# Optimization experiments

Hardware: AMD Instinct MI355X
Metric: run time of the kernel (lower is better)

## Reference

```python
import jax, jax.numpy as jnp
import numpy as np

B, L, F_DIM, H = 4, 384, 640, 128
K_COULOMB = 332.0
DIELECTRIC = 80.0
BN_EPS = 1e-5

# amino-acid charge table, index order 'ACDEFGHIKLMNPQRSTVWY'
_AA = 'ACDEFGHIKLMNPQRSTVWY'
_CHG = {'D': -1.0, 'E': -1.0, 'K': 1.0, 'R': 1.0, 'H': 0.1}
_TABLE = np.zeros((20, 3), dtype=np.float32)
for _i, _aa in enumerate(_AA):
    c = _CHG.get(_aa, 0.0)
    _TABLE[_i, 0 if c > 0 else (1 if c < 0 else 2)] = 1.0
CHG_TABLE = jnp.asarray(_TABLE)


def _conv1d(x, w, b, pad):
    # x: [N, Cin, L], w: [Cout, Cin, K]
    y = jax.lax.conv_general_dilated(x, w, (1,), [(pad, pad)],
                                     dimension_numbers=('NCH', 'OIH', 'NCH'))
    return y + b[None, :, None]


def setup_inputs() -> dict:
    key = jax.random.key(0)
    ks = jax.random.split(key, 32)
    s = 0.05

    def rn(k, shape):
        return (jax.random.normal(k, shape) * s).astype(jnp.float32)

    inp = {
        'features': jax.random.normal(ks[0], (B, L, F_DIM), dtype=jnp.float32),
        'seq_ids': jax.random.randint(ks[1], (B, L), 0, 20, dtype=jnp.int32),
        'structures': (jax.random.normal(ks[2], (B, L, 3)) * 10.0).astype(jnp.float32),
        # charge predictor: Linear(F,H) -> ReLU -> BN(H) -> Linear(H,H//2) -> ReLU -> Linear(H//2,3) -> Softmax
        'W1': rn(ks[3], (F_DIM, H)), 'b1': jnp.zeros((H,), jnp.float32),
        'gamma': jnp.ones((H,), jnp.float32), 'beta': jnp.zeros((H,), jnp.float32),
        'rmean': jnp.zeros((H,), jnp.float32), 'rvar': jnp.ones((H,), jnp.float32),
        'W2': rn(ks[4], (H, H // 2)), 'b2': jnp.zeros((H // 2,), jnp.float32),
        'W3': rn(ks[5], (H // 2, 3)), 'b3': jnp.zeros((3,), jnp.float32),
        # salt bridge detector: Linear(2F+1,H) -> ReLU -> Linear(H,64) -> ReLU -> Linear(64,1) -> Sigmoid
        'sW1': rn(ks[6], (2 * F_DIM + 1, H)), 'sb1': jnp.zeros((H,), jnp.float32),
        'sW2': rn(ks[7], (H, 64)), 'sb2': jnp.zeros((64,), jnp.float32),
        'sW3': rn(ks[8], (64, 1)), 'sb3': jnp.zeros((1,), jnp.float32),
        # potential calculator convs (OIH layout)
        'c1w': rn(ks[9], (16, 1, 5)), 'c1b': jnp.zeros((16,), jnp.float32),
        'c2w': rn(ks[10], (8, 16, 3)), 'c2b': jnp.zeros((8,), jnp.float32),
        'c3w': rn(ks[11], (1, 8, 3)), 'c3b': jnp.zeros((1,), jnp.float32),
    }
    return inp


def reference(features, seq_ids, structures,
              W1, b1, gamma, beta, rmean, rvar, W2, b2, W3, b3,
              sW1, sb1, sW2, sb2, sW3, sb3,
              c1w, c1b, c2w, c2b, c3w, c3b):
    b_, l_, f_ = features.shape

    # true charges from sequence (one-hot pos/neg/neutral)
    true_charges = CHG_TABLE[seq_ids]                               # [B,L,3]

    # --- charge predictor (BatchNorm in eval mode: running stats) ---
    x = features.reshape(-1, f_)
    h = jax.nn.relu(x @ W1 + b1)
    h = gamma * (h - rmean) / jnp.sqrt(rvar + BN_EPS) + beta
    h = jax.nn.relu(h @ W2 + b2)
    pc = jax.nn.softmax(h @ W3 + b3, axis=-1).reshape(b_, l_, 3)    # [B,L,3]

    net_charge = pc[:, :, 0:1] - pc[:, :, 1:2]                      # [B,L,1]

    # --- electrostatic potential: 1D conv stack on [B,1,L] ---
    p = net_charge.transpose(0, 2, 1)                               # [B,1,L]
    p = jax.nn.relu(_conv1d(p, c1w, c1b, 2))
    p = jax.nn.relu(_conv1d(p, c2w, c2b, 1))
    p = _conv1d(p, c3w, c3b, 1)
    potential = p.transpose(0, 2, 1)                                # [B,L,1]

    # --- pairwise distances ---
    diff = structures[:, :, None, :] - structures[:, None, :, :]    # [B,L,L,3]
    D = jnp.sqrt(jnp.sum(diff * diff, axis=-1) + 1e-12)             # [B,L,L]

    # --- salt bridges: vectorized edge-MLP over all (pos i, neg j) pairs ---
    pos = pc[:, :, 0] > pc[:, :, 2]                                 # [B,L]
    neg = pc[:, :, 1] > pc[:, :, 2]                                 # [B,L]
    a, bb, d = sW1[:f_], sW1[f_:2 * f_], sW1[2 * f_]                # split cat([fi,fj,dist]) @ sW1
    fi = features @ a                                               # [B,L,H]
    fj = features @ bb                                              # [B,L,H]
    hid = jax.nn.relu(fi[:, :, None, :] + fj[:, None, :, :] + D[..., None] * d + sb1)  # [B,L,L,H]
    hid2 = jax.nn.relu(hid @ sW2 + sb2)                             # [B,L,L,64]
    prob = jax.nn.sigmoid((hid2 @ sW3 + sb3)[..., 0])               # [B,L,L]
    q = pos[:, :, None] & neg[:, None, :] & (D < 4.0) & (prob > 0.5)
    salt_bridge_masks = (q | q.transpose(0, 2, 1)).astype(jnp.float32)  # [B,L,L]

    # --- Coulomb energy with distance-dependent dielectric ---
    # dielectric = eps * D / 4 -> e_ij = k * q_i q_j / (eps/4 * D^2)
    qc = pc[:, :, 0] - pc[:, :, 1]                                  # [B,L]
    valid = (D < 15.0) & (D > 0.0)
    triu = jnp.triu(jnp.ones((l_, l_), bool), k=1)[None]
    D_safe = jnp.where(valid, D, 1.0)
    e_ij = K_COULOMB * qc[:, :, None] * qc[:, None, :] / ((DIELECTRIC / 4.0) * D_safe * D_safe)
    energy = jnp.sum(jnp.where(valid & triu, e_ij, 0.0), axis=(1, 2))  # [B]

    return (pc, true_charges, net_charge, potential, salt_bridge_masks, energy)
```

## Files before the change

kernel.cpp:

```cpp
#include <hip/hip_runtime.h>

#define LSEQ 384
#define NROWS 1536
#define FDIM 640
#define HDIM 128
#define PART 196608

#define WS_H1P 0
#define WS_FIP (4*PART)
#define WS_FJP (8*PART)
#define WS_FI  (12*PART)
#define WS_FJ  (13*PART)
#define WS_QC  (14*PART)
#define WS_FLAG (WS_QC + NROWS)

#define OUT_PC    0
#define OUT_TC    4608
#define OUT_NET   9216
#define OUT_POT   10752
#define OUT_MASK  12288
#define OUT_EN    602112

__global__ __launch_bounds__(256) void k_gemm(const float* __restrict__ X,
                                              const float* __restrict__ W1,
                                              const float* __restrict__ sW1,
                                              float* __restrict__ ws,
                                              float* __restrict__ out) {
    __shared__ float As[2 * 32 * 34];
    __shared__ float Bs[2 * 32 * 64];
    const int t = threadIdx.x;
    if (blockIdx.x == 0 && blockIdx.y == 0 && blockIdx.z == 0 && t < 4)
        out[OUT_EN + t] = 0.0f;

    const int m0 = blockIdx.x * 32;
    const int gy = blockIdx.y, kz = blockIdx.z;
    const int mat = gy >> 1, half = gy & 1, n0 = half * 64;
    const float* W = (mat == 0) ? W1 : (mat == 1 ? sW1 : sW1 + 640 * 128);
    float* O = ws + (mat == 0 ? WS_H1P : (mat == 1 ? WS_FIP : WS_FJP)) + kz * PART;

    const int a_r = t >> 3, a_c = (t & 7) * 4;
    const int b_r = t >> 4, b_c = (t & 15) * 4;
    const int tx = (t & 15) * 4, ty = (t >> 4) * 2;
    const int k0 = kz * 160;

    float acc[2][4] = {};

    float4 av  = *(const float4*)&X[(m0 + a_r) * FDIM + k0 + a_c];
    float4 bv0 = *(const float4*)&W[(k0 + b_r) * HDIM + n0 + b_c];
    float4 bv1 = *(const float4*)&W[(k0 + b_r + 16) * HDIM + n0 + b_c];
    As[(a_c + 0) * 34 + a_r] = av.x;
    As[(a_c + 1) * 34 + a_r] = av.y;
    As[(a_c + 2) * 34 + a_r] = av.z;
    As[(a_c + 3) * 34 + a_r] = av.w;
    *(float4*)&Bs[b_r * 64 + b_c]        = bv0;
    *(float4*)&Bs[(b_r + 16) * 64 + b_c] = bv1;
    __syncthreads();

    for (int it = 0; it < 5; it++) {
        const int buf = it & 1;
        if (it < 4) {
            const int kk = k0 + (it + 1) * 32;
            av  = *(const float4*)&X[(m0 + a_r) * FDIM + kk + a_c];
            bv0 = *(const float4*)&W[(kk + b_r) * HDIM + n0 + b_c];
            bv1 = *(const float4*)&W[(kk + b_r + 16) * HDIM + n0 + b_c];
        }
        const float* Ab = As + buf * 1088;
        const float* Bb = Bs + buf * 2048;
#pragma unroll
        for (int k = 0; k < 32; k++) {
            float2 a = *(const float2*)&Ab[k * 34 + ty];
            float4 b = *(const float4*)&Bb[k * 64 + tx];
            acc[0][0] = fmaf(a.x, b.x, acc[0][0]);
            acc[0][1] = fmaf(a.x, b.y, acc[0][1]);
            acc[0][2] = fmaf(a.x, b.z, acc[0][2]);
            acc[0][3] = fmaf(a.x, b.w, acc[0][3]);
            acc[1][0] = fmaf(a.y, b.x, acc[1][0]);
            acc[1][1] = fmaf(a.y, b.y, acc[1][1]);
            acc[1][2] = fmaf(a.y, b.z, acc[1][2]);
            acc[1][3] = fmaf(a.y, b.w, acc[1][3]);
        }
        if (it < 4) {
            float* Aw = As + (buf ^ 1) * 1088;
            float* Bw = Bs + (buf ^ 1) * 2048;
            Aw[(a_c + 0) * 34 + a_r] = av.x;
            Aw[(a_c + 1) * 34 + a_r] = av.y;
            Aw[(a_c + 2) * 34 + a_r] = av.z;
            Aw[(a_c + 3) * 34 + a_r] = av.w;
            *(float4*)&Bw[b_r * 64 + b_c]        = bv0;
            *(float4*)&Bw[(b_r + 16) * 64 + b_c] = bv1;
            __syncthreads();
        }
    }
#pragma unroll
    for (int r = 0; r < 2; r++) {
        float4 v = make_float4(acc[r][0], acc[r][1], acc[r][2], acc[r][3]);
        *(float4*)&O[(m0 + ty + r) * HDIM + n0 + tx] = v;
    }
}

__global__ __launch_bounds__(256) void k_row(float* __restrict__ ws,
                                             const float* __restrict__ b1,
                                             const float* __restrict__ gam,
                                             const float* __restrict__ bet,
                                             const float* __restrict__ rmean,
                                             const float* __restrict__ rvar,
                                             const float* __restrict__ W2,
                                             const float* __restrict__ b2,
                                             const float* __restrict__ W3,
                                             const float* __restrict__ b3,
                                             const int* __restrict__ seq,
                                             float* __restrict__ out) {
    const int t = threadIdx.x, w = t >> 6, lane = t & 63;
    const int row = blockIdx.x * 4 + w;
    const long base = (long)row * 128;
    const float* h1p = ws + WS_H1P;
    const float* fip = ws + WS_FIP;
    const float* fjp = ws + WS_FJP;

    {
        float fi0 = fip[base + lane] + fip[PART + base + lane]
                  + fip[2 * PART + base + lane] + fip[3 * PART + base + lane];
        float fi1 = fip[base + 64 + lane] + fip[PART + base + 64 + lane]
                  + fip[2 * PART + base + 64 + lane] + fip[3 * PART + base + 64 + lane];
        float fj0 = fjp[base + lane] + fjp[PART + base + lane]
                  + fjp[2 * PART + base + lane] + fjp[3 * PART + base + lane];
        float fj1 = fjp[base + 64 + lane] + fjp[PART + base + 64 + lane]
                  + fjp[2 * PART + base + 64 + lane] + fjp[3 * PART + base + 64 + lane];
        ws[WS_FI + base + lane]      = fi0;
        ws[WS_FI + base + 64 + lane] = fi1;
        ws[WS_FJ + base + lane]      = fj0;
        ws[WS_FJ + base + 64 + lane] = fj1;
    }

    float h0 = h1p[base + lane] + h1p[PART + base + lane]
             + h1p[2 * PART + base + lane] + h1p[3 * PART + base + lane];
    float h1 = h1p[base + 64 + lane] + h1p[PART + base + 64 + lane]
             + h1p[2 * PART + base + 64 + lane] + h1p[3 * PART + base + 64 + lane];
    h0 = fmaxf(h0 + b1[lane], 0.0f);
    h1 = fmaxf(h1 + b1[64 + lane], 0.0f);
    h0 = gam[lane]      * (h0 - rmean[lane])      / sqrtf(rvar[lane] + 1e-5f)      + bet[lane];
    h1 = gam[64 + lane] * (h1 - rmean[64 + lane]) / sqrtf(rvar[64 + lane] + 1e-5f) + bet[64 + lane];

    float acc = b2[lane];
#pragma unroll
    for (int cc = 0; cc < 64; cc++) {
        float wv0 = W2[cc * 64 + lane];
        float wv1 = W2[(cc + 64) * 64 + lane];
        float hv0 = __uint_as_float(__builtin_amdgcn_readlane(__float_as_uint(h0), cc));
        float hv1 = __uint_as_float(__builtin_amdgcn_readlane(__float_as_uint(h1), cc));
        acc = fmaf(hv0, wv0, acc);
        acc = fmaf(hv1, wv1, acc);
    }
    float h2 = fmaxf(acc, 0.0f);
    float x0 = h2 * W3[lane * 3 + 0];
    float x1 = h2 * W3[lane * 3 + 1];
    float x2 = h2 * W3[lane * 3 + 2];
#pragma unroll
    for (int o = 32; o > 0; o >>= 1) {
        x0 += __shfl_xor(x0, o, 64);
        x1 += __shfl_xor(x1, o, 64);
        x2 += __shfl_xor(x2, o, 64);
    }
    if (lane == 0) {
        float l0 = x0 + b3[0], l1 = x1 + b3[1], l2 = x2 + b3[2];
        float m = fmaxf(l0, fmaxf(l1, l2));
        float e0 = expf(l0 - m), e1 = expf(l1 - m), e2 = expf(l2 - m);
        float s = e0 + e1 + e2;
        float pc0 = e0 / s, pc1 = e1 / s, pc2 = e2 / s;
        out[OUT_PC + row * 3 + 0] = pc0;
        out[OUT_PC + row * 3 + 1] = pc1;
        out[OUT_PC + row * 3 + 2] = pc2;
        float net = pc0 - pc1;
        out[OUT_NET + row] = net;
        ws[WS_QC + row] = net;
        ((int*)(ws + WS_FLAG))[row] = (pc0 > pc2 ? 1 : 0) | (pc1 > pc2 ? 2 : 0);
        int sid = seq[row];
        float c0 = (sid == 6 || sid == 8 || sid == 14) ? 1.0f : 0.0f;
        float c1 = (sid == 2 || sid == 3) ? 1.0f : 0.0f;
        out[OUT_TC + row * 3 + 0] = c0;
        out[OUT_TC + row * 3 + 1] = c1;
        out[OUT_TC + row * 3 + 2] = (c0 == 0.0f && c1 == 0.0f) ? 1.0f : 0.0f;
    }
}

__device__ __forceinline__ float mlp_eval(const float* __restrict__ fi, const float* __restrict__ fj,
                                          int gi, int gj, float D,
                                          float dv0, float dv1, float sb0, float sb1v,
                                          float b2v, float w3l, const float* w2s, int lane) {
    float fi0 = fi[(long)gi * 128 + lane];
    float fi1 = fi[(long)gi * 128 + 64 + lane];
    float fj0 = fj[(long)gj * 128 + lane];
    float fj1 = fj[(long)gj * 128 + 64 + lane];
    float h0 = fmaxf(fi0 + fj0 + D * dv0 + sb0, 0.0f);
    float h1 = fmaxf(fi1 + fj1 + D * dv1 + sb1v, 0.0f);
    float a0 = 0.0f, a1 = 0.0f;
#pragma unroll
    for (int cc = 0; cc < 64; cc++) {
        float hv0 = __uint_as_float(__builtin_amdgcn_readlane(__float_as_uint(h0), cc));
        float hv1 = __uint_as_float(__builtin_amdgcn_readlane(__float_as_uint(h1), cc));
        a0 = fmaf(hv0, w2s[cc * 64 + lane], a0);
        a1 = fmaf(hv1, w2s[(cc + 64) * 64 + lane], a1);
    }
    float x = fmaxf(a0 + a1 + b2v, 0.0f) * w3l;
#pragma unroll
    for (int o = 32; o > 0; o >>= 1) x += __shfl_xor(x, o, 64);
    return x;
}

__global__ __launch_bounds__(256) void k2(const float* __restrict__ S,
                                          const float* __restrict__ ws,
                                          const float* __restrict__ sW1,
                                          const float* __restrict__ sb1,
                                          const float* __restrict__ sW2,
                                          const float* __restrict__ sb2,
                                          const float* __restrict__ sW3,
                                          const float* __restrict__ sb3,
                                          const float* __restrict__ c1w, const float* __restrict__ c1b,
                                          const float* __restrict__ c2w, const float* __restrict__ c2b,
                                          const float* __restrict__ c3w, const float* __restrict__ c3b,
                                          float* __restrict__ out) {
    __shared__ char smem[40960];
    const int t = threadIdx.x;
    const int bi = blockIdx.x;

    if (bi < 4) {
        float* p0 = (float*)smem;
        float* p1 = p0 + 388;
        float* p2 = p1 + 16 * 386;
        const int b = bi;
        for (int j = t; j < LSEQ; j += 256) p0[j + 2] = out[OUT_NET + b * LSEQ + j];
        if (t < 2) { p0[t] = 0.0f; p0[LSEQ + 2 + t] = 0.0f; }
        if (t < 16) { p1[t * 386] = 0.0f; p1[t * 386 + 385] = 0.0f; }
        if (t < 8)  { p2[t * 386] = 0.0f; p2[t * 386 + 385] = 0.0f; }
        __syncthreads();
        for (int pos = t; pos < LSEQ; pos += 256) {
#pragma unroll
            for (int o = 0; o < 16; o++) {
                float acc = c1b[o];
#pragma unroll
                for (int k = 0; k < 5; k++) acc = fmaf(p0[pos + k], c1w[o * 5 + k], acc);
                p1[o * 386 + pos + 1] = fmaxf(acc, 0.0f);
            }
        }
        __syncthreads();
        for (int pos = t; pos < LSEQ; pos += 256) {
#pragma unroll
            for (int o = 0; o < 8; o++) {
                float acc = c2b[o];
                for (int i = 0; i < 16; i++)
#pragma unroll
                    for (int k = 0; k < 3; k++)
                        acc = fmaf(p1[i * 386 + pos + k], c2w[(o * 16 + i) * 3 + k], acc);
                p2[o * 386 + pos + 1] = fmaxf(acc, 0.0f);
            }
        }
        __syncthreads();
        for (int pos = t; pos < LSEQ; pos += 256) {
            float acc = c3b[0];
            for (int i = 0; i < 8; i++)
#pragma unroll
                for (int k = 0; k < 3; k++)
                    acc = fmaf(p2[i * 386 + pos + k], c3w[i * 3 + k], acc);
            out[OUT_POT + b * LSEQ + pos] = acc;
        }
        return;
    }

    float* sx = (float*)smem;
    float* sy = sx + 384;
    float* sz = sy + 384;
    float* sq = sz + 384;
    unsigned int* clist = (unsigned int*)(sz + 768);
    unsigned char* sf = (unsigned char*)(smem + 7680);
    float* red = (float*)(smem + 8064);
    int* cntL = (int*)(smem + 8080);
    float* w2s = (float*)(smem + 8192);

    const float* qc = ws + WS_QC;
    const int* flags = (const int*)(ws + WS_FLAG);
    const float* fi = ws + WS_FI;
    const float* fj = ws + WS_FJ;

    const int row = bi - 4;
    const int b = row / LSEQ;
    const int i = row - b * LSEQ;

    for (int j = t; j < LSEQ; j += 256) {
        int g = b * LSEQ + j;
        sx[j] = S[g * 3 + 0];
        sy[j] = S[g * 3 + 1];
        sz[j] = S[g * 3 + 2];
        sq[j] = qc[g];
        sf[j] = (unsigned char)flags[g];
    }
    if (t == 0) *cntL = 0;
    __syncthreads();

    const float six = sx[i], siy = sy[i], siz = sz[i], qi = sq[i];
    const int fli = sf[i];
    const bool posi = (fli & 1) != 0, negi = (fli & 2) != 0;
    const int lane = t & 63, w = t >> 6;
    float esum = 0.0f;
    float* mrow = out + OUT_MASK + (long)row * LSEQ;

    for (int j = t; j < LSEQ; j += 256) {
        float dx = __fsub_rn(six, sx[j]);
        float dy = __fsub_rn(siy, sy[j]);
        float dz = __fsub_rn(siz, sz[j]);
        float d2 = __fadd_rn(__fadd_rn(__fmul_rn(dx, dx), __fmul_rn(dy, dy)), __fmul_rn(dz, dz));
        d2 = __fadd_rn(d2, 1e-12f);
        float D = __fsqrt_rn(d2);
        mrow[j] = 0.0f;
        if (j > i && D < 15.0f && D > 0.0f) {
            float num = __fmul_rn(__fmul_rn(332.0f, qi), sq[j]);
            float den = __fmul_rn(__fmul_rn(20.0f, D), D);
            esum += __fdiv_rn(num, den);
        }
        int flj = sf[j];
        bool near = (D < 4.0f);
        bool need1 = near && posi && ((flj & 2) != 0);
        bool need2 = near && negi && ((flj & 1) != 0);
        if (need1 || need2) {
            int p = atomicAdd(cntL, 1);
            clist[p] = (unsigned int)j | (need1 ? 512u : 0u) | (need2 ? 1024u : 0u);
        }
    }
#pragma unroll
    for (int o = 32; o > 0; o >>= 1) esum += __shfl_xor(esum, o, 64);
    if (lane == 0) red[w] = esum;
    __syncthreads();
    if (t == 0) {
        float s = red[0] + red[1] + red[2] + red[3];
        atomicAdd(&out[OUT_EN + b], s);
    }

    int nc = *cntL;
    if (nc == 0) return;

    for (int idx = t; idx < 2048; idx += 256)
        ((float4*)w2s)[idx] = ((const float4*)sW2)[idx];
    const float* dvec = sW1 + 1280 * 128;
    const float dv0 = dvec[lane], dv1 = dvec[lane + 64];
    const float sb0 = sb1[lane], sb1v = sb1[lane + 64];
    const float w3l = sW3[lane];
    const float b2v = sb2[lane];
    const float b3v = sb3[0];
    __syncthreads();

    for (int c = w; c < nc; c += 4) {
        unsigned int e = clist[c];
        int j = (int)(e & 511u);
        bool need1 = (e & 512u) != 0, need2 = (e & 1024u) != 0;
        float dx = __fsub_rn(six, sx[j]);
        float dy = __fsub_rn(siy, sy[j]);
        float dz = __fsub_rn(siz, sz[j]);
        float d2 = __fadd_rn(__fadd_rn(__fmul_rn(dx, dx), __fmul_rn(dy, dy)), __fmul_rn(dz, dz));
        d2 = __fadd_rn(d2, 1e-12f);
        float D = __fsqrt_rn(d2);
        int gi = row, gj = b * LSEQ + j;
        bool hit = false;
        if (need1) {
            float x = mlp_eval(fi, fj, gi, gj, D, dv0, dv1, sb0, sb1v, b2v, w3l, w2s, lane);
            hit = (x + b3v) > 0.0f;
        }
        if (!hit && need2) {
            float x = mlp_eval(fi, fj, gj, gi, D, dv0, dv1, sb0, sb1v, b2v, w3l, w2s, lane);
            hit = (x + b3v) > 0.0f;
        }
        if (hit && lane == 0) mrow[j] = 1.0f;
    }
}

extern "C" void kernel_launch(void* const* d_in, const int* in_sizes, int n_in,
                              void* d_out, int out_size, void* d_ws, size_t ws_size,
                              hipStream_t stream) {
    const float* X     = (const float*)d_in[0];
    const int*   seq   = (const int*)d_in[1];
    const float* S     = (const float*)d_in[2];
    const float* W1    = (const float*)d_in[3];
    const float* b1    = (const float*)d_in[4];
    const float* gam   = (const float*)d_in[5];
    const float* bet   = (const float*)d_in[6];
    const float* rmean = (const float*)d_in[7];
    const float* rvar  = (const float*)d_in[8];
    const float* W2    = (const float*)d_in[9];
    const float* b2    = (const float*)d_in[10];
    const float* W3    = (const float*)d_in[11];
    const float* b3    = (const float*)d_in[12];
    const float* sW1   = (const float*)d_in[13];
    const float* sb1   = (const float*)d_in[14];
    const float* sW2   = (const float*)d_in[15];
    const float* sb2   = (const float*)d_in[16];
    const float* sW3   = (const float*)d_in[17];
    const float* sb3   = (const float*)d_in[18];
    const float* c1w   = (const float*)d_in[19];
    const float* c1b   = (const float*)d_in[20];
    const float* c2w   = (const float*)d_in[21];
    const float* c2b   = (const float*)d_in[22];
    const float* c3w   = (const float*)d_in[23];
    const float* c3b   = (const float*)d_in[24];

    float* out = (float*)d_out;
    float* ws  = (float*)d_ws;

    hipLaunchKernelGGL(k_gemm, dim3(48, 6, 4), dim3(256), 0, stream, X, W1, sW1, ws, out);
    hipLaunchKernelGGL(k_row, dim3(384), dim3(256), 0, stream,
                       ws, b1, gam, bet, rmean, rvar, W2, b2, W3, b3, seq, out);
    hipLaunchKernelGGL(k2, dim3(1540), dim3(256), 0, stream,
                       S, ws, sW1, sb1, sW2, sb2, sW3, sb3,
                       c1w, c1b, c2w, c2b, c3w, c3b, out);
}
```

Baseline: 156.1 us.

## Fuse feature GEMM with per-row charge MLP, drop split-K partials

Replaces the split-K GEMM and the separate row-reduction kernel with one fused kernel. Each block computes full-K 8-row tiles for all 128 columns, staging tiles into LDS with global_load_lds. For the charge-predictor matrix it then runs bias/ReLU/BN, the second layer, and softmax in-block. This removes the partial-sum workspace traffic and one kernel launch. The cost is fewer, longer-running blocks (576 blocks of 128 threads with 20 serial K steps), which may lower parallelism and latency hiding.

```diff
diff --git a/kernel.cpp b/kernel.cpp
--- a/kernel.cpp
+++ b/kernel.cpp
@@ -6,9 +6,6 @@
 #define HDIM 128
 #define PART 196608
 
-#define WS_H1P 0
-#define WS_FIP (4*PART)
-#define WS_FJP (8*PART)
 #define WS_FI  (12*PART)
 #define WS_FJ  (13*PART)
 #define WS_QC  (14*PART)
@@ -21,165 +18,158 @@
 #define OUT_MASK  12288
 #define OUT_EN    602112
 
-__global__ __launch_bounds__(256) void k_gemm(const float* __restrict__ X,
-                                              const float* __restrict__ W1,
-                                              const float* __restrict__ sW1,
-                                              float* __restrict__ ws,
-                                              float* __restrict__ out) {
-    __shared__ float As[2 * 32 * 34];
-    __shared__ float Bs[2 * 32 * 64];
-    const int t = threadIdx.x;
-    if (blockIdx.x == 0 && blockIdx.y == 0 && blockIdx.z == 0 && t < 4)
-        out[OUT_EN + t] = 0.0f;
-
-    const int m0 = blockIdx.x * 32;
-    const int gy = blockIdx.y, kz = blockIdx.z;
-    const int mat = gy >> 1, half = gy & 1, n0 = half * 64;
-    const float* W = (mat == 0) ? W1 : (mat == 1 ? sW1 : sW1 + 640 * 128);
-    float* O = ws + (mat == 0 ? WS_H1P : (mat == 1 ? WS_FIP : WS_FJP)) + kz * PART;
-
-    const int a_r = t >> 3, a_c = (t & 7) * 4;
-    const int b_r = t >> 4, b_c = (t & 15) * 4;
-    const int tx = (t & 15) * 4, ty = (t >> 4) * 2;
-    const int k0 = kz * 160;
-
-    float acc[2][4] = {};
-
-    float4 av  = *(const float4*)&X[(m0 + a_r) * FDIM + k0 + a_c];
-    float4 bv0 = *(const float4*)&W[(k0 + b_r) * HDIM + n0 + b_c];
-    float4 bv1 = *(const float4*)&W[(k0 + b_r + 16) * HDIM + n0 + b_c];
-    As[(a_c + 0) * 34 + a_r] = av.x;
-    As[(a_c + 1) * 34 + a_r] = av.y;
-    As[(a_c + 2) * 34 + a_r] = av.z;
-    As[(a_c + 3) * 34 + a_r] = av.w;
-    *(float4*)&Bs[b_r * 64 + b_c]        = bv0;
-    *(float4*)&Bs[(b_r + 16) * 64 + b_c] = bv1;
+typedef float f4 __attribute__((ext_vector_type(4)));
+
+__device__ __forceinline__ void gl16(const float* g, float* l) {
+    __builtin_amdgcn_global_load_lds((const __attribute__((address_space(1))) float*)g,
+                                     (__attribute__((address_space(3))) float*)l, 16, 0, 0);
+}
+
+__global__ __launch_bounds__(128) void k_fused(const float* __restrict__ X,
+                                               const float* __restrict__ W1,
+                                               const float* __restrict__ sW1,
+                                               const float* __restrict__ b1,
+                                               const float* __restrict__ gam,
+                                               const float* __restrict__ bet,
+                                               const float* __restrict__ rmean,
+                                               const float* __restrict__ rvar,
+                                               const float* __restrict__ W2,
+                                               const float* __restrict__ b2,
+                                               const float* __restrict__ W3,
+                                               const float* __restrict__ b3,
+                                               const int* __restrict__ seq,
+                                               float* __restrict__ ws,
+                                               float* __restrict__ out) {
+    __shared__ __align__(16) float As[2][8][32];
+    __shared__ __align__(16) float Bs[2][32][128];
+
+    const int t   = threadIdx.x;
+    const int bx  = blockIdx.x;
+    const int mat = blockIdx.y;
+    const int m0  = bx * 8;
+    const float* W = (mat == 0) ? W1 : (mat == 1 ? sW1 : sW1 + FDIM * HDIM);
+
+    if (mat == 0 && bx == 0 && t < 4) out[OUT_EN + t] = 0.0f;
+
+    const int lane = t & 63, wv = t >> 6;
+    const int rg = t >> 5, cg = t & 31;
+
+    auto stage = [&](int buf, int kt) {
+        const int k0 = kt * 32;
+        const float* wsrc = W + (long)k0 * HDIM;
+        float* bdst = &Bs[buf][0][0];
+#pragma unroll
+        for (int c = 0; c < 8; c++) {
+            const int idx = c * 2 + wv;
+            gl16(wsrc + idx * 256 + lane * 4, bdst + idx * 256);
+        }
+        if (wv == 0)
+            gl16(X + (long)(m0 + (lane >> 3)) * FDIM + k0 + (lane & 7) * 4,
+                 &As[buf][0][0]);
+    };
+
+    f4 acc0 = {0.f, 0.f, 0.f, 0.f};
+    f4 acc1 = {0.f, 0.f, 0.f, 0.f};
+
+    stage(0, 0);
     __syncthreads();
 
-    for (int it = 0; it < 5; it++) {
-        const int buf = it & 1;
-        if (it < 4) {
-            const int kk = k0 + (it + 1) * 32;
-            av  = *(const float4*)&X[(m0 + a_r) * FDIM + kk + a_c];
-            bv0 = *(const float4*)&W[(kk + b_r) * HDIM + n0 + b_c];
-            bv1 = *(const float4*)&W[(kk + b_r + 16) * HDIM + n0 + b_c];
-        }
-        const float* Ab = As + buf * 1088;
-        const float* Bb = Bs + buf * 2048;
-#pragma unroll
-        for (int k = 0; k < 32; k++) {
-            float2 a = *(const float2*)&Ab[k * 34 + ty];
-            float4 b = *(const float4*)&Bb[k * 64 + tx];
-            acc[0][0] = fmaf(a.x, b.x, acc[0][0]);
-            acc[0][1] = fmaf(a.x, b.y, acc[0][1]);
-            acc[0][2] = fmaf(a.x, b.z, acc[0][2]);
-            acc[0][3] = fmaf(a.x, b.w, acc[0][3]);
-            acc[1][0] = fmaf(a.y, b.x, acc[1][0]);
-            acc[1][1] = fmaf(a.y, b.y, acc[1][1]);
-            acc[1][2] = fmaf(a.y, b.z, acc[1][2]);
-            acc[1][3] = fmaf(a.y, b.w, acc[1][3]);
-        }
-        if (it < 4) {
-            float* Aw = As + (buf ^ 1) * 1088;
-            float* Bw = Bs + (buf ^ 1) * 2048;
-            Aw[(a_c + 0) * 34 + a_r] = av.x;
-            Aw[(a_c + 1) * 34 + a_r] = av.y;
-            Aw[(a_c + 2) * 34 + a_r] = av.z;
-            Aw[(a_c + 3) * 34 + a_r] = av.w;
-            *(float4*)&Bw[b_r * 64 + b_c]        = bv0;
-            *(float4*)&Bw[(b_r + 16) * 64 + b_c] = bv1;
-            __syncthreads();
-        }
-    }
-#pragma unroll
-    for (int r = 0; r < 2; r++) {
-        float4 v = make_float4(acc[r][0], acc[r][1], acc[r][2], acc[r][3]);
-        *(float4*)&O[(m0 + ty + r) * HDIM + n0 + tx] = v;
-    }
-}
-
-__global__ __launch_bounds__(256) void k_row(float* __restrict__ ws,
-                                             const float* __restrict__ b1,
-                                             const float* __restrict__ gam,
-                                             const float* __restrict__ bet,
-                                             const float* __restrict__ rmean,
-                                             const float* __restrict__ rvar,
-                                             const float* __restrict__ W2,
-                                             const float* __restrict__ b2,
-                                             const float* __restrict__ W3,
-                                             const float* __restrict__ b3,
-                                             const int* __restrict__ seq,
-                                             float* __restrict__ out) {
-    const int t = threadIdx.x, w = t >> 6, lane = t & 63;
-    const int row = blockIdx.x * 4 + w;
-    const long base = (long)row * 128;
-    const float* h1p = ws + WS_H1P;
-    const float* fip = ws + WS_FIP;
-    const float* fjp = ws + WS_FJP;
-
-    {
-        float fi0 = fip[base + lane] + fip[PART + base + lane]
-                  + fip[2 * PART + base + lane] + fip[3 * PART + base + lane];
-        float fi1 = fip[base + 64 + lane] + fip[PART + base + 64 + lane]
-                  + fip[2 * PART + base + 64 + lane] + fip[3 * PART + base + 64 + lane];
-        float fj0 = fjp[base + lane] + fjp[PART + base + lane]
-                  + fjp[2 * PART + base + lane] + fjp[3 * PART + base + lane];
-        float fj1 = fjp[base + 64 + lane] + fjp[PART + base + 64 + lane]
-                  + fjp[2 * PART + base + 64 + lane] + fjp[3 * PART + base + 64 + lane];
-        ws[WS_FI + base + lane]      = fi0;
-        ws[WS_FI + base + 64 + lane] = fi1;
-        ws[WS_FJ + base + lane]      = fj0;
-        ws[WS_FJ + base + 64 + lane] = fj1;
-    }
-
-    float h0 = h1p[base + lane] + h1p[PART + base + lane]
-             + h1p[2 * PART + base + lane] + h1p[3 * PART + base + lane];
-    float h1 = h1p[base + 64 + lane] + h1p[PART + base + 64 + lane]
-             + h1p[2 * PART + base + 64 + lane] + h1p[3 * PART + base + 64 + lane];
-    h0 = fmaxf(h0 + b1[lane], 0.0f);
-    h1 = fmaxf(h1 + b1[64 + lane], 0.0f);
-    h0 = gam[lane]      * (h0 - rmean[lane])      / sqrtf(rvar[lane] + 1e-5f)      + bet[lane];
-    h1 = gam[64 + lane] * (h1 - rmean[64 + lane]) / sqrtf(rvar[64 + lane] + 1e-5f) + bet[64 + lane];
-
-    float acc = b2[lane];
+#pragma unroll 2
+    for (int kt = 0; kt < 20; kt++) {
+        const int buf = kt & 1;
+        if (kt < 19) stage(buf ^ 1, kt + 1);
+
+        const float* Ab = &As[buf][0][0];
+        const float* Bb = &Bs[buf][0][0];
+#pragma unroll
+        for (int k4 = 0; k4 < 32; k4 += 4) {
+            f4 a0 = *(const f4*)&Ab[(rg * 2 + 0) * 32 + k4];
+            f4 a1 = *(const f4*)&Ab[(rg * 2 + 1) * 32 + k4];
+#pragma unroll
+            for (int kk = 0; kk < 4; kk++) {
+                f4 bv = *(const f4*)&Bb[(k4 + kk) * 128 + cg * 4];
+                acc0 += a0[kk] * bv;
+                acc1 += a1[kk] * bv;
+            }
+        }
+        __syncthreads();
+    }
+
+    if (mat != 0) {
+        float* O = ws + (mat == 1 ? WS_FI : WS_FJ);
+        *(f4*)&O[(long)(m0 + rg * 2 + 0) * HDIM + cg * 4] = acc0;
+        *(f4*)&O[(long)(m0 + rg * 2 + 1) * HDIM + cg * 4] = acc1;
+        return;
+    }
+
+    float* hs = (float*)Bs;
+    *(f4*)&hs[(rg * 2 + 0) * 128 + cg * 4] = acc0;
+    *(f4*)&hs[(rg * 2 + 1) * 128 + cg * 4] = acc1;
+    __syncthreads();
+
+    const float b1v0 = b1[lane],      b1v1 = b1[lane + 64];
+    const float sc0  = gam[lane]      / sqrtf(rvar[lane] + 1e-5f);
+    const float sc1  = gam[lane + 64] / sqrtf(rvar[lane + 64] + 1e-5f);
+    const float rm0  = rmean[lane],   rm1  = rmean[lane + 64];
+    const float bt0  = bet[lane],     bt1  = bet[lane + 64];
+
+    float h0[4], h1[4];
+#pragma unroll
+    for (int r = 0; r < 4; r++) {
+        const int row = wv * 4 + r;
+        float v0 = fmaxf(hs[row * 128 + lane] + b1v0, 0.0f);
+        float v1 = fmaxf(hs[row * 128 + 64 + lane] + b1v1, 0.0f);
+        h0[r] = (v0 - rm0) * sc0 + bt0;
+        h1[r] = (v1 - rm1) * sc1 + bt1;
+    }
+
+    const float b2v = b2[lane];
+    float a2[4] = {b2v, b2v, b2v, b2v};
 #pragma unroll
     for (int cc = 0; cc < 64; cc++) {
-        float wv0 = W2[cc * 64 + lane];
-        float wv1 = W2[(cc + 64) * 64 + lane];
-        float hv0 = __uint_as_float(__builtin_amdgcn_readlane(__float_as_uint(h0), cc));
-        float hv1 = __uint_as_float(__builtin_amdgcn_readlane(__float_as_uint(h1), cc));
-        acc = fmaf(hv0, wv0, acc);
-        acc = fmaf(hv1, wv1, acc);
-    }
-    float h2 = fmaxf(acc, 0.0f);
-    float x0 = h2 * W3[lane * 3 + 0];
-    float x1 = h2 * W3[lane * 3 + 1];
-    float x2 = h2 * W3[lane * 3 + 2];
-#pragma unroll
-    for (int o = 32; o > 0; o >>= 1) {
-        x0 += __shfl_xor(x0, o, 64);
-        x1 += __shfl_xor(x1, o, 64);
-        x2 += __shfl_xor(x2, o, 64);
-    }
-    if (lane == 0) {
-        float l0 = x0 + b3[0], l1 = x1 + b3[1], l2 = x2 + b3[2];
-        float m = fmaxf(l0, fmaxf(l1, l2));
-        float e0 = expf(l0 - m), e1 = expf(l1 - m), e2 = expf(l2 - m);
-        float s = e0 + e1 + e2;
-        float pc0 = e0 / s, pc1 = e1 / s, pc2 = e2 / s;
-        out[OUT_PC + row * 3 + 0] = pc0;
-        out[OUT_PC + row * 3 + 1] = pc1;
-        out[OUT_PC + row * 3 + 2] = pc2;
-        float net = pc0 - pc1;
-        out[OUT_NET + row] = net;
-        ws[WS_QC + row] = net;
-        ((int*)(ws + WS_FLAG))[row] = (pc0 > pc2 ? 1 : 0) | (pc1 > pc2 ? 2 : 0);
-        int sid = seq[row];
-        float c0 = (sid == 6 || sid == 8 || sid == 14) ? 1.0f : 0.0f;
-        float c1 = (sid == 2 || sid == 3) ? 1.0f : 0.0f;
-        out[OUT_TC + row * 3 + 0] = c0;
-        out[OUT_TC + row * 3 + 1] = c1;
-        out[OUT_TC + row * 3 + 2] = (c0 == 0.0f && c1 == 0.0f) ? 1.0f : 0.0f;
+        const float wv0 = W2[cc * 64 + lane];
+        const float wv1 = W2[(cc + 64) * 64 + lane];
+#pragma unroll
+        for (int r = 0; r < 4; r++) {
+            float hv0 = __uint_as_float(__builtin_amdgcn_readlane(__float_as_uint(h0[r]), cc));
+            float hv1 = __uint_as_float(__builtin_amdgcn_readlane(__float_as_uint(h1[r]), cc));
+            a2[r] = fmaf(hv0, wv0, a2[r]);
+            a2[r] = fmaf(hv1, wv1, a2[r]);
+        }
+    }
+
+    const float w30 = W3[lane * 3 + 0], w31 = W3[lane * 3 + 1], w32 = W3[lane * 3 + 2];
+#pragma unroll
+    for (int r = 0; r < 4; r++) {
+        float h2 = fmaxf(a2[r], 0.0f);
+        float x0 = h2 * w30, x1 = h2 * w31, x2 = h2 * w32;
+#pragma unroll
+        for (int o = 32; o > 0; o >>= 1) {
+            x0 += __shfl_xor(x0, o, 64);
+            x1 += __shfl_xor(x1, o, 64);
+            x2 += __shfl_xor(x2, o, 64);
+        }
+        if (lane == 0) {
+            const int row = m0 + wv * 4 + r;
+            float l0 = x0 + b3[0], l1 = x1 + b3[1], l2 = x2 + b3[2];
+            float m = fmaxf(l0, fmaxf(l1, l2));
+            float e0 = expf(l0 - m), e1 = expf(l1 - m), e2 = expf(l2 - m);
+            float s = e0 + e1 + e2;
+            float pc0 = e0 / s, pc1 = e1 / s, pc2 = e2 / s;
+            out[OUT_PC + row * 3 + 0] = pc0;
+            out[OUT_PC + row * 3 + 1] = pc1;
+            out[OUT_PC + row * 3 + 2] = pc2;
+            float net = pc0 - pc1;
+            out[OUT_NET + row] = net;
+            ws[WS_QC + row] = net;
+            ((int*)(ws + WS_FLAG))[row] = (pc0 > pc2 ? 1 : 0) | (pc1 > pc2 ? 2 : 0);
+            int sid = seq[row];
+            float c0 = (sid == 6 || sid == 8 || sid == 14) ? 1.0f : 0.0f;
+            float c1 = (sid == 2 || sid == 3) ? 1.0f : 0.0f;
+            out[OUT_TC + row * 3 + 0] = c0;
+            out[OUT_TC + row * 3 + 1] = c1;
+            out[OUT_TC + row * 3 + 2] = (c0 == 0.0f && c1 == 0.0f) ? 1.0f : 0.0f;
+        }
     }
 }
 
@@ -403,9 +393,8 @@
     float* out = (float*)d_out;
     float* ws  = (float*)d_ws;
 
-    hipLaunchKernelGGL(k_gemm, dim3(48, 6, 4), dim3(256), 0, stream, X, W1, sW1, ws, out);
-    hipLaunchKernelGGL(k_row, dim3(384), dim3(256), 0, stream,
-                       ws, b1, gam, bet, rmean, rvar, W2, b2, W3, b3, seq, out);
+    hipLaunchKernelGGL(k_fused, dim3(192, 3), dim3(128), 0, stream,
+                       X, W1, sW1, b1, gam, bet, rmean, rvar, W2, b2, W3, b3, seq, ws, out);
     hipLaunchKernelGGL(k2, dim3(1540), dim3(256), 0, stream,
                        S, ws, sW1, sb1, sW2, sb2, sW3, sb3,
                        c1w, c1b, c2w, c2b, c3w, c3b, out);
```

Result: slower. 159.7 us (+2.3%).

## Widen GEMM tile to full 128 columns and stage B via global_load_lds

Applied to the files above, without the earlier changes.

The feature-projection GEMM now has each block compute a 32x128 output tile with a 4x4 register tile per thread, instead of two 32x64 tiles in separate blocks. This halves redundant loads of X and doubles the work per block, so the grid shrinks from 1152 to 576 blocks. The weight tiles are copied straight from global memory into LDS with global_load_lds, skipping the register round trip. The costs are lower occupancy and fewer blocks to fill the GPU, plus a dependence on the async LDS load builtin. This GEMM is probably a small share of the total time, which is dominated by the pairwise kernel k2.

```diff
diff --git a/kernel.cpp b/kernel.cpp
--- a/kernel.cpp
+++ b/kernel.cpp
@@ -21,81 +21,91 @@
 #define OUT_MASK  12288
 #define OUT_EN    602112
 
+typedef float f4 __attribute__((ext_vector_type(4)));
+
+__device__ __forceinline__ void gl16(const float* g, float* l) {
+    __builtin_amdgcn_global_load_lds((const __attribute__((address_space(1))) float*)g,
+                                     (__attribute__((address_space(3))) float*)l, 16, 0, 0);
+}
+
 __global__ __launch_bounds__(256) void k_gemm(const float* __restrict__ X,
                                               const float* __restrict__ W1,
                                               const float* __restrict__ sW1,
                                               float* __restrict__ ws,
                                               float* __restrict__ out) {
-    __shared__ float As[2 * 32 * 34];
-    __shared__ float Bs[2 * 32 * 64];
+    __shared__ __align__(16) float As[2][32][36];
+    __shared__ __align__(16) float Bs[2][32][128];
+
     const int t = threadIdx.x;
-    if (blockIdx.x == 0 && blockIdx.y == 0 && blockIdx.z == 0 && t < 4)
+    if (blockIdx.x == 0 && blockIdx.y == 0 && t < 4)
         out[OUT_EN + t] = 0.0f;
 
     const int m0 = blockIdx.x * 32;
-    const int gy = blockIdx.y, kz = blockIdx.z;
-    const int mat = gy >> 1, half = gy & 1, n0 = half * 64;
-    const float* W = (mat == 0) ? W1 : (mat == 1 ? sW1 : sW1 + 640 * 128);
+    const int by = blockIdx.y;
+    const int mat = by >> 2, kz = by & 3;
+    const float* W = (mat == 0) ? W1 : (mat == 1 ? sW1 : sW1 + FDIM * HDIM);
     float* O = ws + (mat == 0 ? WS_H1P : (mat == 1 ? WS_FIP : WS_FJP)) + kz * PART;
-
-    const int a_r = t >> 3, a_c = (t & 7) * 4;
-    const int b_r = t >> 4, b_c = (t & 15) * 4;
-    const int tx = (t & 15) * 4, ty = (t >> 4) * 2;
     const int k0 = kz * 160;
 
-    float acc[2][4] = {};
-
-    float4 av  = *(const float4*)&X[(m0 + a_r) * FDIM + k0 + a_c];
-    float4 bv0 = *(const float4*)&W[(k0 + b_r) * HDIM + n0 + b_c];
-    float4 bv1 = *(const float4*)&W[(k0 + b_r + 16) * HDIM + n0 + b_c];
-    As[(a_c + 0) * 34 + a_r] = av.x;
-    As[(a_c + 1) * 34 + a_r] = av.y;
-    As[(a_c + 2) * 34 + a_r] = av.z;
-    As[(a_c + 3) * 34 + a_r] = av.w;
-    *(float4*)&Bs[b_r * 64 + b_c]        = bv0;
-    *(float4*)&Bs[(b_r + 16) * 64 + b_c] = bv1;
+    const int lane = t & 63, wv = t >> 6;
+    const int rg = t >> 5;
+    const int cg = t & 31;
+    const int ar = t >> 3, ac4 = (t & 7) * 4;
+
+    auto stage_B = [&](int buf, int kk) {
+        const float* src = W + (long)kk * HDIM;
+        float* dst = &Bs[buf][0][0];
+#pragma unroll
+        for (int i = 0; i < 4; i++) {
+            const int c = wv * 4 + i;
+            gl16(src + c * 256 + lane * 4, dst + c * 256);
+        }
+    };
+
+    f4 acc[4];
+    acc[0] = acc[1] = acc[2] = acc[3] = (f4){0.f, 0.f, 0.f, 0.f};
+
+    stage_B(0, k0);
+    {
+        f4 av = *(const f4*)&X[(long)(m0 + ar) * FDIM + k0 + ac4];
+        As[0][ac4 + 0][ar] = av[0];
+        As[0][ac4 + 1][ar] = av[1];
+        As[0][ac4 + 2][ar] = av[2];
+        As[0][ac4 + 3][ar] = av[3];
+    }
     __syncthreads();
 
-    for (int it = 0; it < 5; it++) {
-        const int buf = it & 1;
-        if (it < 4) {
-            const int kk = k0 + (it + 1) * 32;
-            av  = *(const float4*)&X[(m0 + a_r) * FDIM + kk + a_c];
-            bv0 = *(const float4*)&W[(kk + b_r) * HDIM + n0 + b_c];
-            bv1 = *(const float4*)&W[(kk + b_r + 16) * HDIM + n0 + b_c];
-        }
-        const float* Ab = As + buf * 1088;
-        const float* Bb = Bs + buf * 2048;
+    for (int kt = 0; kt < 5; kt++) {
+        const int buf = kt & 1;
+        f4 av;
+        if (kt < 4) {
+            const int kk = k0 + (kt + 1) * 32;
+            stage_B(buf ^ 1, kk);
+            av = *(const f4*)&X[(long)(m0 + ar) * FDIM + kk + ac4];
+        }
+        const float* Ab = &As[buf][0][0];
+        const float* Bb = &Bs[buf][0][0];
 #pragma unroll
         for (int k = 0; k < 32; k++) {
-            float2 a = *(const float2*)&Ab[k * 34 + ty];
-            float4 b = *(const float4*)&Bb[k * 64 + tx];
-            acc[0][0] = fmaf(a.x, b.x, acc[0][0]);
-            acc[0][1] = fmaf(a.x, b.y, acc[0][1]);
-            acc[0][2] = fmaf(a.x, b.z, acc[0][2]);
-            acc[0][3] = fmaf(a.x, b.w, acc[0][3]);
-            acc[1][0] = fmaf(a.y, b.x, acc[1][0]);
-            acc[1][1] = fmaf(a.y, b.y, acc[1][1]);
-            acc[1][2] = fmaf(a.y, b.z, acc[1][2]);
-            acc[1][3] = fmaf(a.y, b.w, acc[1][3]);
-        }
-        if (it < 4) {
-            float* Aw = As + (buf ^ 1) * 1088;
-            float* Bw = Bs + (buf ^ 1) * 2048;
-            Aw[(a_c + 0) * 34 + a_r] = av.x;
-            Aw[(a_c + 1) * 34 + a_r] = av.y;
-            Aw[(a_c + 2) * 34 + a_r] = av.z;
-            Aw[(a_c + 3) * 34 + a_r] = av.w;
-            *(float4*)&Bw[b_r * 64 + b_c]        = bv0;
-            *(float4*)&Bw[(b_r + 16) * 64 + b_c] = bv1;
-            __syncthreads();
-        }
-    }
-#pragma unroll
-    for (int r = 0; r < 2; r++) {
-        float4 v = make_float4(acc[r][0], acc[r][1], acc[r][2], acc[r][3]);
-        *(float4*)&O[(m0 + ty + r) * HDIM + n0 + tx] = v;
-    }
+            f4 a = *(const f4*)&Ab[k * 36 + rg * 4];
+            f4 b = *(const f4*)&Bb[k * 128 + cg * 4];
+            acc[0] += a[0] * b;
+            acc[1] += a[1] * b;
+            acc[2] += a[2] * b;
+            acc[3] += a[3] * b;
+        }
+        if (kt < 4) {
+            As[(buf ^ 1)][ac4 + 0][ar] = av[0];
+            As[(buf ^ 1)][ac4 + 1][ar] = av[1];
+            As[(buf ^ 1)][ac4 + 2][ar] = av[2];
+            As[(buf ^ 1)][ac4 + 3][ar] = av[3];
+        }
+        __syncthreads();
+    }
+
+#pragma unroll
+    for (int r = 0; r < 4; r++)
+        *(f4*)&O[(long)(m0 + rg * 4 + r) * HDIM + cg * 4] = acc[r];
 }
 
 __global__ __launch_bounds__(256) void k_row(float* __restrict__ ws,
@@ -403,7 +413,7 @@
     float* out = (float*)d_out;
     float* ws  = (float*)d_ws;
 
-    hipLaunchKernelGGL(k_gemm, dim3(48, 6, 4), dim3(256), 0, stream, X, W1, sW1, ws, out);
+    hipLaunchKernelGGL(k_gemm, dim3(48, 12), dim3(256), 0, stream, X, W1, sW1, ws, out);
     hipLaunchKernelGGL(k_row, dim3(384), dim3(256), 0, stream,
                        ws, b1, gam, bet, rmean, rvar, W2, b2, W3, b3, seq, out);
     hipLaunchKernelGGL(k2, dim3(1540), dim3(256), 0, stream,
```

Result: slower. 161.2 us (+3.2%).
